# Performance work log

Hardware: AMD Instinct MI355X
Metric: run time of the kernel (lower is better)

## Reference

```python
import jax, jax.numpy as jnp
import numpy as np

D = 256        # input_dim / embed_dim
H = 128        # hidden_dim
NH = 8         # attention heads
S = 64         # number of superpoint segments
LN_EPS = 1e-5
CW = 0.3       # consistency weight


def layernorm(x, g, b):
    m = jnp.mean(x, axis=-1, keepdims=True)
    v = jnp.var(x, axis=-1, keepdims=True)
    return (x - m) * jax.lax.rsqrt(v + LN_EPS) * g + b


def mlp(x, w1, b1, g1, be1, w2, b2, g2, be2):
    # Linear -> LayerNorm -> ReLU -> Linear -> LayerNorm (torch Sequential)
    h = jax.nn.relu(layernorm(x @ w1.T + b1, g1, be1))
    return layernorm(h @ w2.T + b2, g2, be2)


def setup_inputs() -> dict:
    key = jax.random.key(0)
    ks = jax.random.split(key, 16)
    B, N = 2, 512
    p = {}
    p['coordinates'] = jax.random.normal(ks[0], (B, N, 3), dtype=jnp.float32)
    p['features'] = jax.random.normal(ks[1], (B, N, D), dtype=jnp.float32)
    p['superpoint_labels'] = jax.random.randint(ks[2], (B, N), 0, S, dtype=jnp.int32)
    sc = 0.02
    # geometric_encoder: Linear(9,H), LN(H), ReLU, Linear(H,D), LN(D)
    p['ge_w1'] = jax.random.normal(ks[3], (H, 9), dtype=jnp.float32) * sc
    p['ge_b1'] = jnp.zeros((H,), jnp.float32)
    p['ge_g1'] = jnp.ones((H,), jnp.float32)
    p['ge_be1'] = jnp.zeros((H,), jnp.float32)
    p['ge_w2'] = jax.random.normal(ks[4], (D, H), dtype=jnp.float32) * sc
    p['ge_b2'] = jnp.zeros((D,), jnp.float32)
    p['ge_g2'] = jnp.ones((D,), jnp.float32)
    p['ge_be2'] = jnp.zeros((D,), jnp.float32)
    # superpoint_aggregator: Linear(D,H), LN(H), ReLU, Linear(H,D), LN(D)
    p['ag_w1'] = jax.random.normal(ks[5], (H, D), dtype=jnp.float32) * sc
    p['ag_b1'] = jnp.zeros((H,), jnp.float32)
    p['ag_g1'] = jnp.ones((H,), jnp.float32)
    p['ag_be1'] = jnp.zeros((H,), jnp.float32)
    p['ag_w2'] = jax.random.normal(ks[6], (D, H), dtype=jnp.float32) * sc
    p['ag_b2'] = jnp.zeros((D,), jnp.float32)
    p['ag_g2'] = jnp.ones((D,), jnp.float32)
    p['ag_be2'] = jnp.zeros((D,), jnp.float32)
    # MultiheadAttention projections (torch [out,in] layout)
    p['wq'] = jax.random.normal(ks[7], (D, D), dtype=jnp.float32) * sc
    p['bq'] = jnp.zeros((D,), jnp.float32)
    p['wk'] = jax.random.normal(ks[8], (D, D), dtype=jnp.float32) * sc
    p['bk'] = jnp.zeros((D,), jnp.float32)
    p['wv'] = jax.random.normal(ks[9], (D, D), dtype=jnp.float32) * sc
    p['bv'] = jnp.zeros((D,), jnp.float32)
    p['wo'] = jax.random.normal(ks[10], (D, D), dtype=jnp.float32) * sc
    p['bo'] = jnp.zeros((D,), jnp.float32)
    return p


def reference(coordinates, features, superpoint_labels,
              ge_w1, ge_b1, ge_g1, ge_be1, ge_w2, ge_b2, ge_g2, ge_be2,
              ag_w1, ag_b1, ag_g1, ag_be1, ag_w2, ag_b2, ag_g2, ag_be2,
              wq, bq, wk, bk, wv, bv, wo, bo):
    B, N, Dm = features.shape
    # pairwise geometric features [B,N,N,*]
    rel = coordinates[:, :, None, :] - coordinates[:, None, :, :]
    dist = jnp.linalg.norm(rel, axis=-1, keepdims=True)
    rn = rel / jnp.maximum(dist, 1e-12)  # F.normalize semantics
    r0, r1, r2 = rn[..., 0], rn[..., 1], rn[..., 2]
    z = jnp.zeros_like(r0)
    # torch code writes to channels -2, -1, 2 of 5 => [0, 0, r1*r2, r0*r1, r0*r2]
    ang = jnp.stack([z, z, r1 * r2, r0 * r1, r0 * r2], axis=-1)
    geo_rel = jnp.concatenate([dist, rn, ang], axis=-1)  # [B,N,N,9]
    enc = mlp(geo_rel, ge_w1, ge_b1, ge_g1, ge_be1, ge_w2, ge_b2, ge_g2, ge_be2)
    geo_ctx = jnp.mean(enc, axis=2)  # [B,N,D]

    # vectorized per-superpoint segment mean + aggregator + scatter-back
    def per_batch(feat, geo, lab):
        ones = jnp.ones(lab.shape, feat.dtype)
        cnt = jax.ops.segment_sum(ones, lab, num_segments=S)          # [S]
        denom = jnp.maximum(cnt, 1.0)[:, None]
        mf = jax.ops.segment_sum(feat, lab, num_segments=S) / denom  # [S,D]
        mg = jax.ops.segment_sum(geo, lab, num_segments=S) / denom   # [S,D]
        agg = mlp(mf, ag_w1, ag_b1, ag_g1, ag_be1, ag_w2, ag_b2, ag_g2, ag_be2)
        comb = agg + mg
        upd = (1.0 - CW) * feat + CW * comb[lab]
        keep = (cnt >= 2.0)[lab][:, None]  # groups with <2 points untouched
        return jnp.where(keep, upd, feat)

    enhanced = jax.vmap(per_batch)(features, geo_ctx, superpoint_labels)

    # MultiheadAttention(q=enhanced, k=v=geo_ctx)
    hd = Dm // NH
    scale = np.float32(1.0 / np.sqrt(hd))
    q = (enhanced @ wq.T + bq).reshape(B, N, NH, hd).transpose(0, 2, 1, 3)
    k = (geo_ctx @ wk.T + bk).reshape(B, N, NH, hd).transpose(0, 2, 1, 3)
    v = (geo_ctx @ wv.T + bv).reshape(B, N, NH, hd).transpose(0, 2, 1, 3)
    attn = jax.nn.softmax(jnp.einsum('bhqd,bhkd->bhqk', q, k) * scale, axis=-1)
    o = jnp.einsum('bhqk,bhkd->bhqd', attn, v).transpose(0, 2, 1, 3).reshape(B, N, Dm)
    spatial = o @ wo.T + bo
    return enhanced + 0.5 * spatial
```

## Files before the change

### kernel.cpp

```cpp
#include <hip/hip_runtime.h>

#define NPTS 512
#define DIM  256
#define HID  128
#define NSEG 64
#define LN_EPS 1e-5f
#define KTS 520

typedef short s16x4 __attribute__((ext_vector_type(4)));
typedef short s16x8 __attribute__((ext_vector_type(8)));
typedef float f32x4 __attribute__((ext_vector_type(4)));
typedef const float* fpc;

__device__ __forceinline__ unsigned short f2bf(float f) {
  unsigned int u = __builtin_bit_cast(unsigned int, f);
  u += 0x7FFFu + ((u >> 16) & 1u);
  return (unsigned short)(u >> 16);
}

__global__ void k02_prep_agg(
    fpc ge_w1, fpc ge_b1, fpc ge_w2, fpc ge_b2,
    fpc features, const int* __restrict__ labels,
    fpc wk, fpc wv, fpc wq, fpc wo,
    fpc ag_w1, fpc ag_b1, fpc ag_g1, fpc ag_be1,
    fpc ag_w2, fpc ag_b2, fpc ag_g2, fpc ag_be2,
    unsigned short* __restrict__ gmw, float* __restrict__ uw,
    float* __restrict__ tvw, float* __restrict__ scw, float* __restrict__ qfw,
    float* __restrict__ wkT, float* __restrict__ wvT,
    float* __restrict__ wqT, float* __restrict__ woT,
    float* __restrict__ comb, float* __restrict__ cntf, float* __restrict__ mgsum)
{
  const int blk = blockIdx.x;
  const int t = threadIdx.x;
  if (blk < 130) {
    if (t < 128) {
      if (blk < 128) {
        const int c = blk;
        float acc = 0.f;
        for (int d = 0; d < DIM; ++d) acc += ge_w2[d * HID + c] * ge_w2[d * HID + t];
        gmw[c * HID + t] = f2bf(acc);
      } else if (blk == 128) {
        float uu = 0.f, tv = 0.f;
        for (int d = 0; d < DIM; ++d) { const float w = ge_w2[d * HID + t]; uu += w; tv += ge_b2[d] * w; }
        uw[t] = uu; tvw[t] = tv;
        if (t == 0) {
          float s = 0.f, s2 = 0.f;
          for (int d = 0; d < DIM; ++d) { const float bb = ge_b2[d]; s += bb; s2 += bb * bb; }
          scw[0] = s; scw[1] = s2;
        }
      } else {
        if (t < 101) {
          float acc = 0.f;
          if (t < 81) {
            const int a = t / 9, c = t % 9;
            for (int h = 0; h < HID; ++h) acc += ge_w1[h * 9 + a] * ge_w1[h * 9 + c];
            qfw[a * 12 + c] = acc;
          } else if (t < 90) {
            const int a = t - 81;
            for (int h = 0; h < HID; ++h) acc += ge_w1[h * 9 + a];
            qfw[108 + a] = acc;
          } else if (t < 99) {
            const int a = t - 90;
            for (int h = 0; h < HID; ++h) acc += ge_b1[h] * ge_w1[h * 9 + a];
            qfw[117 + a] = acc;
          } else if (t == 99) {
            float acc2 = 0.f;
            for (int h = 0; h < HID; ++h) acc2 += ge_b1[h];
            qfw[126] = acc2;
          } else {
            float acc2 = 0.f;
            for (int h = 0; h < HID; ++h) acc2 += ge_b1[h] * ge_b1[h];
            qfw[127] = acc2;
          }
        }
      }
    }
    return;
  }
  if (blk < 162) {
    __shared__ __align__(16) float T[32][256];
    const int tr = blk - 130;
    const int m = tr >> 3;
    fpc src = (m == 0) ? wk : (m == 1) ? wv : (m == 2) ? wq : wo;
    float* dst = (m == 0) ? wkT : (m == 1) ? wvT : (m == 2) ? wqT : woT;
    const int c0 = (tr & 7) * 32;
    for (int i = 0; i < 32; ++i) T[i][t] = src[(c0 + i) * DIM + t];
    __syncthreads();
    #pragma unroll
    for (int j4 = 0; j4 < 32; j4 += 4) {
      f32x4 v;
      v[0] = T[j4 + 0][t]; v[1] = T[j4 + 1][t];
      v[2] = T[j4 + 2][t]; v[3] = T[j4 + 3][t];
      *(f32x4*)&dst[t * DIM + c0 + j4] = v;
    }
    return;
  }
  const int item = blk - 162;
  const int lane = t & 63;
  const int wid = t >> 6;
  const int b = item >> 6;
  const int s = item & 63;
  __shared__ __align__(16) int labS[NPTS];
  __shared__ __align__(16) float mfS[DIM];
  __shared__ __align__(16) float h1S[HID];
  __shared__ __align__(16) float red[8];
  mgsum[(b * NSEG + s) * DIM + t] = 0.f;
  for (int n = t; n < NPTS; n += 256) labS[n] = labels[b * NPTS + n];
  __syncthreads();
  float accf = 0.f;
  int cnt = 0;
  for (int n = 0; n < NPTS; n += 4) {
    const int4 l4 = *(const int4*)&labS[n];
    if (l4.x == s) { cnt++; accf += features[(b * NPTS + n + 0) * DIM + t]; }
    if (l4.y == s) { cnt++; accf += features[(b * NPTS + n + 1) * DIM + t]; }
    if (l4.z == s) { cnt++; accf += features[(b * NPTS + n + 2) * DIM + t]; }
    if (l4.w == s) { cnt++; accf += features[(b * NPTS + n + 3) * DIM + t]; }
  }
  const float denom = fmaxf((float)cnt, 1.f);
  mfS[t] = accf / denom;
  __syncthreads();
  float hval = 0.f;
  if (t < HID) {
    float o = ag_b1[t];
    for (int k = 0; k < DIM; k += 4) {
      const f32x4 x = *(const f32x4*)&mfS[k];
      const f32x4 w = *(const f32x4*)&ag_w1[t * DIM + k];
      o += x[0] * w[0] + x[1] * w[1] + x[2] * w[2] + x[3] * w[3];
    }
    hval = o;
  }
  float sv = (t < HID) ? hval : 0.f;
  float qv = (t < HID) ? hval * hval : 0.f;
  #pragma unroll
  for (int off = 1; off < 64; off <<= 1) { sv += __shfl_xor(sv, off); qv += __shfl_xor(qv, off); }
  if (lane == 0 && wid < 2) { red[wid * 2] = sv; red[wid * 2 + 1] = qv; }
  __syncthreads();
  if (t < HID) {
    const float s1 = red[0] + red[2], q1 = red[1] + red[3];
    const float mean = s1 * (1.f / 128.f);
    const float var = fmaxf(q1 * (1.f / 128.f) - mean * mean, 0.f);
    const float rs = rsqrtf(var + LN_EPS);
    h1S[t] = fmaxf((hval - mean) * rs * ag_g1[t] + ag_be1[t], 0.f);
  }
  __syncthreads();
  float o = ag_b2[t];
  for (int k = 0; k < HID; k += 4) {
    const f32x4 x = *(const f32x4*)&h1S[k];
    const f32x4 w = *(const f32x4*)&ag_w2[t * HID + k];
    o += x[0] * w[0] + x[1] * w[1] + x[2] * w[2] + x[3] * w[3];
  }
  float sv2 = o, qv2 = o * o;
  #pragma unroll
  for (int off = 1; off < 64; off <<= 1) { sv2 += __shfl_xor(sv2, off); qv2 += __shfl_xor(qv2, off); }
  if (lane == 0) { red[wid * 2] = sv2; red[wid * 2 + 1] = qv2; }
  __syncthreads();
  const float sa = red[0] + red[2] + red[4] + red[6];
  const float qa = red[1] + red[3] + red[5] + red[7];
  const float mean = sa * (1.f / 256.f);
  const float var = fmaxf(qa * (1.f / 256.f) - mean * mean, 0.f);
  const float rs = rsqrtf(var + LN_EPS);
  comb[(b * NSEG + s) * DIM + t] = (o - mean) * rs * ag_g2[t] + ag_be2[t];
  if (t == 0) cntf[b * NSEG + s] = (float)cnt;
}

__global__ __launch_bounds__(256, 4) void k1_geo(
    fpc coords, const int* __restrict__ labels,
    fpc g1, fpc be1, fpc w1, fpc b1,
    fpc w2, fpc b2, fpc g2, fpc be2,
    fpc wkT, fpc bk, fpc wvT, fpc bv,
    const unsigned short* __restrict__ gmw, fpc uw, fpc tvw, fpc scw, fpc qfw,
    float* __restrict__ Kt, float* __restrict__ Vout, float* __restrict__ mgsum)
{
  const int t = threadIdx.x;
  const int lane = t & 63;
  const int wid = t >> 6;
  const int bi = blockIdx.x;
  const int b = bi >> 9;

  __shared__ __align__(16) float xs[NPTS][8];
  __shared__ __align__(16) float st[NPTS][2];
  __shared__ __align__(16) float qf[128];
  __shared__ __align__(16) unsigned short h1s[32][136];
  __shared__ __align__(16) float red2[32][12];
  __shared__ __align__(16) float haS[128];
  __shared__ __align__(16) float gS[256];
  __shared__ float srsS, srmS;

  if (t < 128) qf[t] = qfw[t];

  float w1r[2][7], b1r[2], g1r[2], be1r[2];
  #pragma unroll
  for (int r = 0; r < 2; ++r) {
    const int hh = lane * 2 + r;
    w1r[r][0] = w1[hh * 9 + 0]; w1r[r][1] = w1[hh * 9 + 1];
    w1r[r][2] = w1[hh * 9 + 2]; w1r[r][3] = w1[hh * 9 + 3];
    w1r[r][4] = w1[hh * 9 + 6]; w1r[r][5] = w1[hh * 9 + 7];
    w1r[r][6] = w1[hh * 9 + 8];
    b1r[r] = b1[hh]; g1r[r] = g1[hh]; be1r[r] = be1[hh];
  }
  const int n16 = lane & 15;
  const int q16 = lane >> 4;
  const int colc0 = wid * 32 + n16;
  s16x8 gfrag[2][4];
  float u_c[2], tv_c[2];
  #pragma unroll
  for (int dt = 0; dt < 2; ++dt) {
    const int c = colc0 + dt * 16;
    u_c[dt] = uw[c];
    tv_c[dt] = 2.f * tvw[c];
    #pragma unroll
    for (int kt = 0; kt < 4; ++kt)
      gfrag[dt][kt] = *(const s16x8*)&gmw[c * HID + kt * 32 + q16 * 8];
  }
  const float sb = scw[0], sb2 = scw[1];
  const float cix = coords[bi * 3 + 0];
  const float ciy = coords[bi * 3 + 1];
  const float ciz = coords[bi * 3 + 2];
  __syncthreads();

  #pragma unroll
  for (int jj = 0; jj < 2; ++jj) {
    const int j = t + jj * 256;
    const float cjx = coords[(b * NPTS + j) * 3 + 0];
    const float cjy = coords[(b * NPTS + j) * 3 + 1];
    const float cjz = coords[(b * NPTS + j) * 3 + 2];
    const float rx = cix - cjx, ry = ciy - cjy, rz = ciz - cjz;
    const float dist = sqrtf(rx * rx + ry * ry + rz * rz);
    const float inv = 1.f / fmaxf(dist, 1e-12f);
    const float r0 = rx * inv, r1 = ry * inv, r2 = rz * inv;
    const float x0 = dist, x1 = r0, x2 = r1, x3 = r2;
    const float x6 = r1 * r2, x7 = r0 * r1, x8 = r0 * r2;
    float S1 = qf[126] + qf[108] * x0 + qf[109] * x1 + qf[110] * x2 + qf[111] * x3
             + qf[114] * x6 + qf[115] * x7 + qf[116] * x8;
    float tx = qf[117] * x0 + qf[118] * x1 + qf[119] * x2 + qf[120] * x3
             + qf[123] * x6 + qf[124] * x7 + qf[125] * x8;
    const float xv[9] = {x0, x1, x2, x3, 0.f, 0.f, x6, x7, x8};
    float quad = 0.f;
    #pragma unroll
    for (int a = 0; a < 9; ++a) {
      if (a == 4 || a == 5) continue;
      const f32x4 q0 = *(const f32x4*)&qf[a * 12];
      const f32x4 q1 = *(const f32x4*)&qf[a * 12 + 4];
      const f32x4 q2 = *(const f32x4*)&qf[a * 12 + 8];
      const float ya = q0[0] * x0 + q0[1] * x1 + q0[2] * x2 + q0[3] * x3
                     + q1[2] * x6 + q1[3] * x7 + q2[0] * x8;
      quad += ya * xv[a];
    }
    const float S2 = quad + 2.f * tx + qf[127];
    const float mean = S1 * (1.f / 128.f);
    const float var = fmaxf(S2 * (1.f / 128.f) - mean * mean, 0.f);
    st[j][0] = mean;
    st[j][1] = rsqrtf(var + LN_EPS);
    f32x4 X0; X0[0] = x0; X0[1] = x1; X0[2] = x2; X0[3] = x3;
    f32x4 X1; X1[0] = x6; X1[1] = x7; X1[2] = x8; X1[3] = 0.f;
    *(f32x4*)&xs[j][0] = X0;
    *(f32x4*)&xs[j][4] = X1;
  }
  __syncthreads();

  float haL[2] = {0.f, 0.f};
  float srs = 0.f, srm = 0.f;
  const bool own = (wid == 0) && (n16 == 0);

  for (int jb = 0; jb < NPTS; jb += 32) {
    #pragma unroll
    for (int sr = 0; sr < 8; ++sr) {
      const int m = sr * 4 + wid;
      const int j = jb + m;
      const f32x4 X0 = *(const f32x4*)&xs[j][0];
      const f32x4 X1 = *(const f32x4*)&xs[j][4];
      const float2 ms = *(const float2*)&st[j][0];
      unsigned int pk = 0;
      #pragma unroll
      for (int r = 0; r < 2; ++r) {
        const float a = b1r[r]
          + X0[0] * w1r[r][0] + X0[1] * w1r[r][1] + X0[2] * w1r[r][2] + X0[3] * w1r[r][3]
          + X1[0] * w1r[r][4] + X1[1] * w1r[r][5] + X1[2] * w1r[r][6];
        const float e = (a - ms.x) * ms.y * g1r[r] + be1r[r];
        pk |= ((unsigned int)f2bf(fmaxf(e, 0.f))) << (16 * r);
      }
      *(unsigned int*)&h1s[m][lane * 2] = pk;
    }
    __syncthreads();
    f32x4 acc2[2][2];
    #pragma unroll
    for (int mt = 0; mt < 2; ++mt)
      #pragma unroll
      for (int dt = 0; dt < 2; ++dt) {
        f32x4 z; z[0] = tv_c[dt]; z[1] = tv_c[dt]; z[2] = tv_c[dt]; z[3] = tv_c[dt];
        acc2[mt][dt] = z;
      }
    #pragma unroll
    for (int mt = 0; mt < 2; ++mt)
      #pragma unroll
      for (int kt = 0; kt < 4; ++kt) {
        const s16x8 af = *(const s16x8*)&h1s[mt * 16 + n16][kt * 32 + q16 * 8];
        #pragma unroll
        for (int dt = 0; dt < 2; ++dt)
          acc2[mt][dt] = __builtin_amdgcn_mfma_f32_16x16x32_bf16(af, gfrag[dt][kt], acc2[mt][dt], 0, 0, 0);
      }
    float h1v[2][2][4];
    #pragma unroll
    for (int mt = 0; mt < 2; ++mt)
      #pragma unroll
      for (int dt = 0; dt < 2; ++dt)
        #pragma unroll
        for (int r = 0; r < 4; ++r) {
          const unsigned short hv = h1s[mt * 16 + q16 * 4 + r][colc0 + dt * 16];
          h1v[mt][dt][r] = __builtin_bit_cast(float, ((unsigned int)hv) << 16);
        }
    #pragma unroll
    for (int mt = 0; mt < 2; ++mt) {
      float sR[4], qR[4];
      #pragma unroll
      for (int r = 0; r < 4; ++r) {
        sR[r] = u_c[0] * h1v[mt][0][r] + u_c[1] * h1v[mt][1][r];
        qR[r] = acc2[mt][0][r] * h1v[mt][0][r] + acc2[mt][1][r] * h1v[mt][1][r];
      }
      #pragma unroll
      for (int off = 1; off < 16; off <<= 1)
        #pragma unroll
        for (int r = 0; r < 4; ++r) {
          sR[r] += __shfl_xor(sR[r], off);
          qR[r] += __shfl_xor(qR[r], off);
        }
      if (n16 == 0)
        #pragma unroll
        for (int r = 0; r < 4; ++r) {
          red2[mt * 16 + q16 * 4 + r][wid * 2 + 0] = sR[r];
          red2[mt * 16 + q16 * 4 + r][wid * 2 + 1] = qR[r];
        }
    }
    __syncthreads();
    #pragma unroll
    for (int mt = 0; mt < 2; ++mt)
      #pragma unroll
      for (int r = 0; r < 4; ++r) {
        const int row = mt * 16 + q16 * 4 + r;
        const f32x4 p0 = *(const f32x4*)&red2[row][0];
        const f32x4 p1 = *(const f32x4*)&red2[row][4];
        const float s = p0[0] + p0[2] + p1[0] + p1[2];
        const float q = p0[1] + p0[3] + p1[1] + p1[3];
        const float mean = (s + sb) * (1.f / 256.f);
        const float var = fmaxf((q + sb2) * (1.f / 256.f) - mean * mean, 0.f);
        const float rs = rsqrtf(var + LN_EPS);
        haL[0] += rs * h1v[mt][0][r];
        haL[1] += rs * h1v[mt][1][r];
        if (own) { srs += rs; srm += rs * mean; }
      }
  }

  haL[0] += __shfl_xor(haL[0], 16); haL[0] += __shfl_xor(haL[0], 32);
  haL[1] += __shfl_xor(haL[1], 16); haL[1] += __shfl_xor(haL[1], 32);
  float sa = srs, sm = srm;
  sa += __shfl_xor(sa, 16); sa += __shfl_xor(sa, 32);
  sm += __shfl_xor(sm, 16); sm += __shfl_xor(sm, 32);
  if (t == 0) { srsS = sa; srmS = sm; }
  if (lane < 16) { haS[colc0] = haL[0]; haS[colc0 + 16] = haL[1]; }
  __syncthreads();
  const float srsT = srsS, srmT = srmS;
  float dot = 0.f;
  for (int k = 0; k < HID; k += 4) {
    const f32x4 w = *(const f32x4*)&w2[t * HID + k];
    const f32x4 h = *(const f32x4*)&haS[k];
    dot += w[0] * h[0] + w[1] * h[1] + w[2] * h[2] + w[3] * h[3];
  }
  const float gv = (dot + b2[t] * srsT - srmT) * (1.f / 512.f) * g2[t] + be2[t];
  gS[t] = gv;
  const int l = labels[bi];
  atomicAdd(&mgsum[(b * NSEG + l) * DIM + t], gv);
  __syncthreads();
  float kacc = bk[t], vacc = bv[t];
  for (int k = 0; k < DIM; k += 4) {
    const f32x4 g4 = *(const f32x4*)&gS[k];
    kacc += g4[0] * wkT[(k + 0) * DIM + t] + g4[1] * wkT[(k + 1) * DIM + t]
          + g4[2] * wkT[(k + 2) * DIM + t] + g4[3] * wkT[(k + 3) * DIM + t];
    vacc += g4[0] * wvT[(k + 0) * DIM + t] + g4[1] * wvT[(k + 1) * DIM + t]
          + g4[2] * wvT[(k + 2) * DIM + t] + g4[3] * wvT[(k + 3) * DIM + t];
  }
  Kt[((b * 8 + (t >> 5)) * 32 + (t & 31)) * KTS + (bi & 511)] = kacc;
  Vout[bi * DIM + t] = vacc;
}

__global__ __launch_bounds__(256, 4) void k5_fused(
    fpc features, const int* __restrict__ labels,
    fpc comb, fpc cntf, fpc mgsum,
    fpc Kt, fpc V, fpc wqT, fpc bq, fpc woT, fpc bo,
    float* __restrict__ out)
{
  const int row = blockIdx.x;
  const int b = row >> 9;
  const int t = threadIdx.x;
  const int w = t >> 6;
  const int l = t & 63;
  __shared__ __align__(16) float E[256];
  __shared__ __align__(16) float Qs[256];
  __shared__ __align__(16) float Px[4][512];
  __shared__ __align__(16) float OcS[256];

  {
    const int lab = labels[row];
    const float cn = cntf[b * NSEG + lab];
    const float f = features[row * DIM + t];
    float v = f;
    if (cn >= 2.f) {
      const float ag = comb[(b * NSEG + lab) * DIM + t];
      const float mg = mgsum[(b * NSEG + lab) * DIM + t];
      v = 0.7f * f + 0.3f * (ag + mg / cn);
    }
    E[t] = v;
  }
  __syncthreads();
  {
    const int c4 = w * 64 + (l & 15) * 4;
    const int k0 = (l >> 4) * 64;
    f32x4 q4 = {0.f, 0.f, 0.f, 0.f};
    for (int k = k0; k < k0 + 64; ++k) {
      const float e = E[k];
      const f32x4 wv4 = *(const f32x4*)&wqT[k * DIM + c4];
      #pragma unroll
      for (int i = 0; i < 4; ++i) q4[i] += e * wv4[i];
    }
    #pragma unroll
    for (int i = 0; i < 4; ++i) { q4[i] += __shfl_xor(q4[i], 16); q4[i] += __shfl_xor(q4[i], 32); }
    if (l < 16) {
      const f32x4 bq4 = *(const f32x4*)&bq[c4];
      f32x4 o;
      #pragma unroll
      for (int i = 0; i < 4; ++i) o[i] = q4[i] + bq4[i];
      *(f32x4*)&Qs[c4] = o;
    }
  }
  for (int hi = 0; hi < 2; ++hi) {
    const int h = w * 2 + hi;
    f32x4 s4[2] = {{0.f, 0.f, 0.f, 0.f}, {0.f, 0.f, 0.f, 0.f}};
    const long kbase = (long)((b * 8 + h) * 32) * KTS;
    for (int d = 0; d < 32; ++d) {
      const float qd = Qs[h * 32 + d];
      const fpc kr = &Kt[kbase + (long)d * KTS];
      const f32x4 k0v = *(const f32x4*)&kr[l * 4];
      const f32x4 k1v = *(const f32x4*)&kr[256 + l * 4];
      #pragma unroll
      for (int i = 0; i < 4; ++i) { s4[0][i] += qd * k0v[i]; s4[1][i] += qd * k1v[i]; }
    }
    #pragma unroll
    for (int i = 0; i < 4; ++i) {
      s4[0][i] *= 0.1767766952966369f;
      s4[1][i] *= 0.1767766952966369f;
    }
    float mx = s4[0][0];
    #pragma unroll
    for (int i = 1; i < 4; ++i) mx = fmaxf(mx, s4[0][i]);
    #pragma unroll
    for (int i = 0; i < 4; ++i) mx = fmaxf(mx, s4[1][i]);
    #pragma unroll
    for (int off = 1; off < 64; off <<= 1) mx = fmaxf(mx, __shfl_xor(mx, off));
    f32x4 p0, p1;
    float sum = 0.f;
    #pragma unroll
    for (int i = 0; i < 4; ++i) { p0[i] = __expf(s4[0][i] - mx); sum += p0[i]; }
    #pragma unroll
    for (int i = 0; i < 4; ++i) { p1[i] = __expf(s4[1][i] - mx); sum += p1[i]; }
    #pragma unroll
    for (int off = 1; off < 64; off <<= 1) sum += __shfl_xor(sum, off);
    const float ri = 1.f / sum;
    #pragma unroll
    for (int i = 0; i < 4; ++i) { p0[i] *= ri; p1[i] *= ri; }
    *(f32x4*)&Px[w][l * 4] = p0;
    *(f32x4*)&Px[w][256 + l * 4] = p1;
    const int j2 = (l & 15) * 2;
    const int k0 = (l >> 4) * 128;
    float o0 = 0.f, o1 = 0.f;
    for (int k = k0; k < k0 + 128; ++k) {
      const float pv = Px[w][k];
      const float2 vv = *(const float2*)&V[(b * NPTS + k) * DIM + h * 32 + j2];
      o0 += pv * vv.x; o1 += pv * vv.y;
    }
    o0 += __shfl_xor(o0, 16); o1 += __shfl_xor(o1, 16);
    o0 += __shfl_xor(o0, 32); o1 += __shfl_xor(o1, 32);
    if (l < 16) { OcS[h * 32 + j2] = o0; OcS[h * 32 + j2 + 1] = o1; }
  }
  __syncthreads();
  {
    const int c4 = w * 64 + (l & 15) * 4;
    const int j0 = (l >> 4) * 64;
    f32x4 d4 = {0.f, 0.f, 0.f, 0.f};
    for (int j = j0; j < j0 + 64; ++j) {
      const float oc = OcS[j];
      const f32x4 wv4 = *(const f32x4*)&woT[j * DIM + c4];
      #pragma unroll
      for (int i = 0; i < 4; ++i) d4[i] += oc * wv4[i];
    }
    #pragma unroll
    for (int i = 0; i < 4; ++i) { d4[i] += __shfl_xor(d4[i], 16); d4[i] += __shfl_xor(d4[i], 32); }
    if (l < 16) {
      const f32x4 bo4 = *(const f32x4*)&bo[c4];
      const f32x4 e4 = *(const f32x4*)&E[c4];
      f32x4 o;
      #pragma unroll
      for (int i = 0; i < 4; ++i) o[i] = e4[i] + 0.5f * (d4[i] + bo4[i]);
      *(f32x4*)&out[row * DIM + c4] = o;
    }
  }
}

extern "C" void kernel_launch(void* const* d_in, const int* in_sizes, int n_in,
                              void* d_out, int out_size, void* d_ws, size_t ws_size,
                              hipStream_t stream)
{
  fpc coords  = (fpc)d_in[0];
  fpc features= (fpc)d_in[1];
  const int* labels = (const int*)d_in[2];
  fpc ge_w1 = (fpc)d_in[3],  ge_b1 = (fpc)d_in[4],  ge_g1 = (fpc)d_in[5],  ge_be1 = (fpc)d_in[6];
  fpc ge_w2 = (fpc)d_in[7],  ge_b2 = (fpc)d_in[8],  ge_g2 = (fpc)d_in[9],  ge_be2 = (fpc)d_in[10];
  fpc ag_w1 = (fpc)d_in[11], ag_b1 = (fpc)d_in[12], ag_g1 = (fpc)d_in[13], ag_be1 = (fpc)d_in[14];
  fpc ag_w2 = (fpc)d_in[15], ag_b2 = (fpc)d_in[16], ag_g2 = (fpc)d_in[17], ag_be2 = (fpc)d_in[18];
  fpc wq = (fpc)d_in[19], bq = (fpc)d_in[20];
  fpc wk = (fpc)d_in[21], bk = (fpc)d_in[22];
  fpc wv = (fpc)d_in[23], bv = (fpc)d_in[24];
  fpc wo = (fpc)d_in[25], bo = (fpc)d_in[26];

  float* ws = (float*)d_ws;
  float* comb    = ws;
  float* cntf    = comb + 32768;
  float* Vb      = cntf + 128;
  float* Ktb     = Vb + 262144;
  float* mgsum   = Ktb + 266240;
  float* gmwF    = mgsum + 32768;
  float* uw      = gmwF + 8192;
  float* tvw     = uw + 128;
  float* scw     = tvw + 128;
  float* qfw     = scw + 8;
  float* wkT     = qfw + 128;
  float* wvT     = wkT + 65536;
  float* wqT     = wvT + 65536;
  float* woT     = wqT + 65536;

  k02_prep_agg<<<290, 256, 0, stream>>>(ge_w1, ge_b1, ge_w2, ge_b2,
                                        features, labels, wk, wv, wq, wo,
                                        ag_w1, ag_b1, ag_g1, ag_be1,
                                        ag_w2, ag_b2, ag_g2, ag_be2,
                                        (unsigned short*)gmwF, uw, tvw, scw, qfw,
                                        wkT, wvT, wqT, woT, comb, cntf, mgsum);
  k1_geo<<<1024, 256, 0, stream>>>(coords, labels, ge_g1, ge_be1, ge_w1, ge_b1,
                                   ge_w2, ge_b2, ge_g2, ge_be2,
                                   wkT, bk, wvT, bv,
                                   (const unsigned short*)gmwF, uw, tvw, scw, qfw,
                                   Ktb, Vb, mgsum);
  k5_fused<<<1024, 256, 0, stream>>>(features, labels, comb, cntf, mgsum,
                                     Ktb, Vb, wqT, bq, woT, bo, (float*)d_out);
}
```

Baseline: 323.9 us.

## Double k1_geo block to 512 threads, splitting MFMA row tiles and K/V projections

The geometric-encoder kernel now launches 512 threads per block instead of 256. Each of the 8 waves handles one 16-row MFMA tile and one column group, where previously each wave handled two row tiles. The per-point K and V projections are split so that half the threads compute K and the other half compute V. This is meant to raise per-block parallelism and cut serial work per wave, at the cost of an extra shared-memory reduction, an extra barrier, and possibly lower occupancy from the larger blocks.

Result: no change. 323.1 us (median of 2 runs) (-0.3%).

```diff
diff --git a/kernel.cpp b/kernel.cpp
--- a/kernel.cpp
+++ b/kernel.cpp
@@ -163,7 +163,7 @@
   if (t == 0) cntf[b * NSEG + s] = (float)cnt;
 }
 
-__global__ __launch_bounds__(256, 4) void k1_geo(
+__global__ __launch_bounds__(512, 4) void k1_geo(
     fpc coords, const int* __restrict__ labels,
     fpc g1, fpc be1, fpc w1, fpc b1,
     fpc w2, fpc b2, fpc g2, fpc be2,
@@ -173,7 +173,9 @@
 {
   const int t = threadIdx.x;
   const int lane = t & 63;
-  const int wid = t >> 6;
+  const int w = t >> 6;
+  const int mtw = w >> 2;
+  const int cg = w & 3;
   const int bi = blockIdx.x;
   const int b = bi >> 9;
 
@@ -182,9 +184,9 @@
   __shared__ __align__(16) float qf[128];
   __shared__ __align__(16) unsigned short h1s[32][136];
   __shared__ __align__(16) float red2[32][12];
-  __shared__ __align__(16) float haS[128];
+  __shared__ __align__(16) float haS[2][128];
   __shared__ __align__(16) float gS[256];
-  __shared__ float srsS, srmS;
+  __shared__ float srsP[2], srmP[2];
 
   if (t < 128) qf[t] = qfw[t];
 
@@ -200,7 +202,7 @@
   }
   const int n16 = lane & 15;
   const int q16 = lane >> 4;
-  const int colc0 = wid * 32 + n16;
+  const int colc0 = cg * 32 + n16;
   s16x8 gfrag[2][4];
   float u_c[2], tv_c[2];
   #pragma unroll
@@ -218,9 +220,8 @@
   const float ciz = coords[bi * 3 + 2];
   __syncthreads();
 
-  #pragma unroll
-  for (int jj = 0; jj < 2; ++jj) {
-    const int j = t + jj * 256;
+  {
+    const int j = t;
     const float cjx = coords[(b * NPTS + j) * 3 + 0];
     const float cjy = coords[(b * NPTS + j) * 3 + 1];
     const float cjz = coords[(b * NPTS + j) * 3 + 2];
@@ -260,12 +261,12 @@
 
   float haL[2] = {0.f, 0.f};
   float srs = 0.f, srm = 0.f;
-  const bool own = (wid == 0) && (n16 == 0);
+  const bool own = (cg == 0) && (n16 == 0);
 
   for (int jb = 0; jb < NPTS; jb += 32) {
     #pragma unroll
-    for (int sr = 0; sr < 8; ++sr) {
-      const int m = sr * 4 + wid;
+    for (int sr = 0; sr < 4; ++sr) {
+      const int m = sr * 8 + w;
       const int j = jb + m;
       const f32x4 X0 = *(const f32x4*)&xs[j][0];
       const f32x4 X1 = *(const f32x4*)&xs[j][4];
@@ -282,72 +283,61 @@
       *(unsigned int*)&h1s[m][lane * 2] = pk;
     }
     __syncthreads();
-    f32x4 acc2[2][2];
-    #pragma unroll
-    for (int mt = 0; mt < 2; ++mt)
-      #pragma unroll
-      for (int dt = 0; dt < 2; ++dt) {
-        f32x4 z; z[0] = tv_c[dt]; z[1] = tv_c[dt]; z[2] = tv_c[dt]; z[3] = tv_c[dt];
-        acc2[mt][dt] = z;
+    f32x4 acc2[2];
+    #pragma unroll
+    for (int dt = 0; dt < 2; ++dt) {
+      f32x4 z; z[0] = tv_c[dt]; z[1] = tv_c[dt]; z[2] = tv_c[dt]; z[3] = tv_c[dt];
+      acc2[dt] = z;
+    }
+    #pragma unroll
+    for (int kt = 0; kt < 4; ++kt) {
+      const s16x8 af = *(const s16x8*)&h1s[mtw * 16 + n16][kt * 32 + q16 * 8];
+      #pragma unroll
+      for (int dt = 0; dt < 2; ++dt)
+        acc2[dt] = __builtin_amdgcn_mfma_f32_16x16x32_bf16(af, gfrag[dt][kt], acc2[dt], 0, 0, 0);
+    }
+    float h1v[2][4];
+    #pragma unroll
+    for (int dt = 0; dt < 2; ++dt)
+      #pragma unroll
+      for (int r = 0; r < 4; ++r) {
+        const unsigned short hv = h1s[mtw * 16 + q16 * 4 + r][colc0 + dt * 16];
+        h1v[dt][r] = __builtin_bit_cast(float, ((unsigned int)hv) << 16);
       }
-    #pragma unroll
-    for (int mt = 0; mt < 2; ++mt)
-      #pragma unroll
-      for (int kt = 0; kt < 4; ++kt) {
-        const s16x8 af = *(const s16x8*)&h1s[mt * 16 + n16][kt * 32 + q16 * 8];
-        #pragma unroll
-        for (int dt = 0; dt < 2; ++dt)
-          acc2[mt][dt] = __builtin_amdgcn_mfma_f32_16x16x32_bf16(af, gfrag[dt][kt], acc2[mt][dt], 0, 0, 0);
+    float sR[4], qR[4];
+    #pragma unroll
+    for (int r = 0; r < 4; ++r) {
+      sR[r] = u_c[0] * h1v[0][r] + u_c[1] * h1v[1][r];
+      qR[r] = acc2[0][r] * h1v[0][r] + acc2[1][r] * h1v[1][r];
+    }
+    #pragma unroll
+    for (int off = 1; off < 16; off <<= 1)
+      #pragma unroll
+      for (int r = 0; r < 4; ++r) {
+        sR[r] += __shfl_xor(sR[r], off);
+        qR[r] += __shfl_xor(qR[r], off);
       }
-    float h1v[2][2][4];
-    #pragma unroll
-    for (int mt = 0; mt < 2; ++mt)
-      #pragma unroll
-      for (int dt = 0; dt < 2; ++dt)
-        #pragma unroll
-        for (int r = 0; r < 4; ++r) {
-          const unsigned short hv = h1s[mt * 16 + q16 * 4 + r][colc0 + dt * 16];
-          h1v[mt][dt][r] = __builtin_bit_cast(float, ((unsigned int)hv) << 16);
-        }
-    #pragma unroll
-    for (int mt = 0; mt < 2; ++mt) {
-      float sR[4], qR[4];
+    if (n16 == 0)
       #pragma unroll
       for (int r = 0; r < 4; ++r) {
-        sR[r] = u_c[0] * h1v[mt][0][r] + u_c[1] * h1v[mt][1][r];
-        qR[r] = acc2[mt][0][r] * h1v[mt][0][r] + acc2[mt][1][r] * h1v[mt][1][r];
+        red2[mtw * 16 + q16 * 4 + r][cg * 2 + 0] = sR[r];
+        red2[mtw * 16 + q16 * 4 + r][cg * 2 + 1] = qR[r];
       }
-      #pragma unroll
-      for (int off = 1; off < 16; off <<= 1)
-        #pragma unroll
-        for (int r = 0; r < 4; ++r) {
-          sR[r] += __shfl_xor(sR[r], off);
-          qR[r] += __shfl_xor(qR[r], off);
-        }
-      if (n16 == 0)
-        #pragma unroll
-        for (int r = 0; r < 4; ++r) {
-          red2[mt * 16 + q16 * 4 + r][wid * 2 + 0] = sR[r];
-          red2[mt * 16 + q16 * 4 + r][wid * 2 + 1] = qR[r];
-        }
-    }
     __syncthreads();
     #pragma unroll
-    for (int mt = 0; mt < 2; ++mt)
-      #pragma unroll
-      for (int r = 0; r < 4; ++r) {
-        const int row = mt * 16 + q16 * 4 + r;
-        const f32x4 p0 = *(const f32x4*)&red2[row][0];
-        const f32x4 p1 = *(const f32x4*)&red2[row][4];
-        const float s = p0[0] + p0[2] + p1[0] + p1[2];
-        const float q = p0[1] + p0[3] + p1[1] + p1[3];
-        const float mean = (s + sb) * (1.f / 256.f);
-        const float var = fmaxf((q + sb2) * (1.f / 256.f) - mean * mean, 0.f);
-        const float rs = rsqrtf(var + LN_EPS);
-        haL[0] += rs * h1v[mt][0][r];
-        haL[1] += rs * h1v[mt][1][r];
-        if (own) { srs += rs; srm += rs * mean; }
-      }
+    for (int r = 0; r < 4; ++r) {
+      const int row = mtw * 16 + q16 * 4 + r;
+      const f32x4 p0 = *(const f32x4*)&red2[row][0];
+      const f32x4 p1 = *(const f32x4*)&red2[row][4];
+      const float s = p0[0] + p0[2] + p1[0] + p1[2];
+      const float q = p0[1] + p0[3] + p1[1] + p1[3];
+      const float mean = (s + sb) * (1.f / 256.f);
+      const float var = fmaxf((q + sb2) * (1.f / 256.f) - mean * mean, 0.f);
+      const float rs = rsqrtf(var + LN_EPS);
+      haL[0] += rs * h1v[0][r];
+      haL[1] += rs * h1v[1][r];
+      if (own) { srs += rs; srm += rs * mean; }
+    }
   }
 
   haL[0] += __shfl_xor(haL[0], 16); haL[0] += __shfl_xor(haL[0], 32);
@@ -355,31 +345,43 @@
   float sa = srs, sm = srm;
   sa += __shfl_xor(sa, 16); sa += __shfl_xor(sa, 32);
   sm += __shfl_xor(sm, 16); sm += __shfl_xor(sm, 32);
-  if (t == 0) { srsS = sa; srmS = sm; }
-  if (lane < 16) { haS[colc0] = haL[0]; haS[colc0 + 16] = haL[1]; }
-  __syncthreads();
-  const float srsT = srsS, srmT = srmS;
-  float dot = 0.f;
-  for (int k = 0; k < HID; k += 4) {
-    const f32x4 w = *(const f32x4*)&w2[t * HID + k];
-    const f32x4 h = *(const f32x4*)&haS[k];
-    dot += w[0] * h[0] + w[1] * h[1] + w[2] * h[2] + w[3] * h[3];
-  }
-  const float gv = (dot + b2[t] * srsT - srmT) * (1.f / 512.f) * g2[t] + be2[t];
-  gS[t] = gv;
-  const int l = labels[bi];
-  atomicAdd(&mgsum[(b * NSEG + l) * DIM + t], gv);
-  __syncthreads();
-  float kacc = bk[t], vacc = bv[t];
-  for (int k = 0; k < DIM; k += 4) {
-    const f32x4 g4 = *(const f32x4*)&gS[k];
-    kacc += g4[0] * wkT[(k + 0) * DIM + t] + g4[1] * wkT[(k + 1) * DIM + t]
-          + g4[2] * wkT[(k + 2) * DIM + t] + g4[3] * wkT[(k + 3) * DIM + t];
-    vacc += g4[0] * wvT[(k + 0) * DIM + t] + g4[1] * wvT[(k + 1) * DIM + t]
-          + g4[2] * wvT[(k + 2) * DIM + t] + g4[3] * wvT[(k + 3) * DIM + t];
-  }
-  Kt[((b * 8 + (t >> 5)) * 32 + (t & 31)) * KTS + (bi & 511)] = kacc;
-  Vout[bi * DIM + t] = vacc;
+  if (lane == 0 && cg == 0) { srsP[mtw] = sa; srmP[mtw] = sm; }
+  if (lane < 16) { haS[mtw][colc0] = haL[0]; haS[mtw][colc0 + 16] = haL[1]; }
+  __syncthreads();
+  if (t < 128) haS[0][t] += haS[1][t];
+  __syncthreads();
+  const float srsT = srsP[0] + srsP[1];
+  const float srmT = srmP[0] + srmP[1];
+  if (t < 256) {
+    float dot = 0.f;
+    for (int k = 0; k < HID; k += 4) {
+      const f32x4 wv4 = *(const f32x4*)&w2[t * HID + k];
+      const f32x4 h = *(const f32x4*)&haS[0][k];
+      dot += wv4[0] * h[0] + wv4[1] * h[1] + wv4[2] * h[2] + wv4[3] * h[3];
+    }
+    const float gv = (dot + b2[t] * srsT - srmT) * (1.f / 512.f) * g2[t] + be2[t];
+    gS[t] = gv;
+    atomicAdd(&mgsum[(b * NSEG + labels[bi]) * DIM + t], gv);
+  }
+  __syncthreads();
+  if (t < 256) {
+    float kacc = bk[t];
+    for (int k = 0; k < DIM; k += 4) {
+      const f32x4 g4 = *(const f32x4*)&gS[k];
+      kacc += g4[0] * wkT[(k + 0) * DIM + t] + g4[1] * wkT[(k + 1) * DIM + t]
+            + g4[2] * wkT[(k + 2) * DIM + t] + g4[3] * wkT[(k + 3) * DIM + t];
+    }
+    Kt[((b * 8 + (t >> 5)) * 32 + (t & 31)) * KTS + (bi & 511)] = kacc;
+  } else {
+    const int c = t - 256;
+    float vacc = bv[c];
+    for (int k = 0; k < DIM; k += 4) {
+      const f32x4 g4 = *(const f32x4*)&gS[k];
+      vacc += g4[0] * wvT[(k + 0) * DIM + c] + g4[1] * wvT[(k + 1) * DIM + c]
+            + g4[2] * wvT[(k + 2) * DIM + c] + g4[3] * wvT[(k + 3) * DIM + c];
+    }
+    Vout[bi * DIM + c] = vacc;
+  }
 }
 
 __global__ __launch_bounds__(256, 4) void k5_fused(
@@ -542,7 +544,7 @@
                                         ag_w2, ag_b2, ag_g2, ag_be2,
                                         (unsigned short*)gmwF, uw, tvw, scw, qfw,
                                         wkT, wvT, wqT, woT, comb, cntf, mgsum);
-  k1_geo<<<1024, 256, 0, stream>>>(coords, labels, ge_g1, ge_be1, ge_w1, ge_b1,
+  k1_geo<<<1024, 512, 0, stream>>>(coords, labels, ge_g1, ge_be1, ge_w1, ge_b1,
                                    ge_w2, ge_b2, ge_g2, ge_be2,
                                    wkT, bk, wvT, bv,
                                    (const unsigned short*)gmwF, uw, tvw, scw, qfw,
```
